# Kernel optimization log

Measured on AMD Instinct MI355X. Metric: run time of the kernel, lower is better.

The kernel has to match this reference:

```python
import jax, jax.numpy as jnp
import numpy as np

B, C, H, W = 32, 256, 32, 32
NUM_EMB = 1024
BETA = 0.25  # commitment_loss_weight


def setup_inputs() -> dict:
    key = jax.random.key(0)
    k_u, k_cb = jax.random.split(key)
    u = jax.random.normal(k_u, (B, C, H, W), dtype=jnp.float32)
    # kaiming_normal_ fan_in, relu: std = sqrt(2 / fan_in), fan_in = embedding_dim
    cb_std = float(np.sqrt(2.0 / C))
    codebook = jax.random.normal(k_cb, (NUM_EMB, C), dtype=jnp.float32) * cb_std
    return {"u": u, "codebook": codebook}


def reference(u, codebook):
    # u: [B, C, H, W] -> flat: [B*H*W, C]
    flat = jnp.transpose(u, (0, 2, 3, 1)).reshape(-1, C)
    # squared euclidean distances (argmin-equivalent to torch.cdist)
    d = (
        jnp.sum(flat * flat, axis=1, keepdims=True)
        - 2.0 * flat @ codebook.T
        + jnp.sum(codebook * codebook, axis=1)[None, :]
    )  # [B*H*W, NUM_EMB]
    encoding_indices = jnp.argmin(d, axis=1)  # [B*H*W]
    z_q = codebook[encoding_indices].reshape(B, H, W, C)
    z_q = jnp.transpose(z_q, (0, 3, 1, 2))  # [B, C, H, W]
    # straight-through (note: z_q is NOT detached here, matching the source)
    z_train = z_q + (u - jax.lax.stop_gradient(u))
    codebook_loss = jnp.mean((z_q - jax.lax.stop_gradient(u)) ** 2)
    commitment_loss = jnp.mean((u - jax.lax.stop_gradient(z_q)) ** 2)
    vq_loss = codebook_loss + BETA * commitment_loss
    return u, z_train, vq_loss, encoding_indices.reshape(B, H, W)
```

## Files before the change

kernel.cpp:

```cpp
#include <hip/hip_runtime.h>
#include <hip/hip_bf16.h>

#define BATCH 32
#define CHN   256
#define HWSZ  1024
#define NPIX  32768
#define NEMB  1024
#define NELEM 8388608
#define FLT_BIG 3.402823466e+38f

#define WS_CBT   0
#define WS_CNORM 262144
#define WS_XNORM 263168
#define WS_ACCUM 295936

#define OUT_U    0
#define OUT_ZT   8388608
#define OUT_LOSS 16777216
#define OUT_IDX  16777217

__device__ __forceinline__ void gld_lds16(const float* g, float* lds) {
    __builtin_amdgcn_global_load_lds(
        (const __attribute__((address_space(1))) void*)g,
        (__attribute__((address_space(3))) void*)lds, 16, 0, 0);
}

__global__ __launch_bounds__(256) void k_prep_cb(const float* __restrict__ cb,
                                                 float* __restrict__ ws) {
    int n = blockIdx.x;
    int c = threadIdx.x;
    float v = cb[(size_t)n * CHN + c];
    ws[WS_CBT + (size_t)c * NEMB + n] = v;
    float s = v * v;
    #pragma unroll
    for (int off = 32; off > 0; off >>= 1) s += __shfl_down(s, off, 64);
    __shared__ float ls[4];
    int w = threadIdx.x >> 6;
    if ((threadIdx.x & 63) == 0) ls[w] = s;
    __syncthreads();
    if (threadIdx.x == 0) ws[WS_CNORM + n] = (ls[0] + ls[1]) + (ls[2] + ls[3]);
}

__global__ __launch_bounds__(256) void k_prep_x(const float* __restrict__ u,
                                                float* __restrict__ ws) {
    int P0   = blockIdx.x * 64;
    int b    = P0 / HWSZ;
    int hw0  = P0 % HWSZ;
    int lane = threadIdx.x & 63;
    int grp  = threadIdx.x >> 6;
    const float* up = u + (size_t)b * CHN * HWSZ + hw0 + lane;
    float s = 0.f;
    int cbase = grp * 64;
    #pragma unroll 8
    for (int c = 0; c < 64; ++c) {
        float v = up[(size_t)(cbase + c) * HWSZ];
        s = fmaf(v, v, s);
    }
    __shared__ float ls[4][64];
    ls[grp][lane] = s;
    __syncthreads();
    if (grp == 0) {
        float x = (ls[0][lane] + ls[1][lane]) + (ls[2][lane] + ls[3][lane]);
        ws[WS_XNORM + P0 + lane] = x;
    }
    if (blockIdx.x == 0 && threadIdx.x == 0)
        *(double*)&ws[WS_ACCUM] = 0.0;
}

__global__ __launch_bounds__(256, 2) void k_argmin(const float* __restrict__ u,
                                                   const float* __restrict__ ws,
                                                   float* __restrict__ out_idx) {
    __shared__ float s_u[2][32][64];
    __shared__ float s_cb[2][32][256];

    const float* cbT   = ws + WS_CBT;
    const float* cnorm = ws + WS_CNORM;
    const float* xnorm = ws + WS_XNORM;

    int T   = blockIdx.x;
    int P0  = T * 64;
    int b   = P0 / HWSZ;
    int hw0 = P0 % HWSZ;
    int tid = threadIdx.x;
    int tx  = tid & 7;
    int ty  = tid >> 3;

    const float* ub = u + (size_t)b * CHN * HWSZ + hw0;

    int uq0_k  = tid >> 4;
    int uq0_p  = (tid & 15) << 2;
    int uq1_k  = (256 + tid) >> 4;
    int uq1_p  = (tid & 15) << 2;
    int cb_k0  = tid >> 6;
    int cb_j   = (tid & 63) << 2;

    float xn[8];
    #pragma unroll
    for (int i = 0; i < 8; ++i) xn[i] = xnorm[P0 + tx * 8 + i];

    float dmin[8];
    int   imin[8];
    #pragma unroll
    for (int i = 0; i < 8; ++i) { dmin[i] = FLT_BIG; imin[i] = 0; }

    auto stage = [&](int s, int buf) {
        int nt = s >> 3;
        int kc = s & 7;
        int n0 = nt * 256;
        int c0 = kc * 32;
        float* su  = &s_u[buf][0][0];
        float* scb = &s_cb[buf][0][0];
        gld_lds16(&ub[(size_t)(c0 + uq0_k) * HWSZ + uq0_p], &su[tid * 4]);
        gld_lds16(&ub[(size_t)(c0 + uq1_k) * HWSZ + uq1_p], &su[(256 + tid) * 4]);
        #pragma unroll
        for (int it = 0; it < 8; ++it) {
            int k = cb_k0 + it * 4;
            gld_lds16(&cbT[(size_t)(c0 + k) * NEMB + n0 + cb_j],
                      &scb[(it * 256 + tid) * 4]);
        }
    };

    stage(0, 0);

    for (int nt = 0; nt < 4; ++nt) {
        int n0 = nt * 256;
        float acc[8][8];
        #pragma unroll
        for (int i = 0; i < 8; ++i)
            #pragma unroll
            for (int j = 0; j < 8; ++j) acc[i][j] = 0.f;

        for (int kc = 0; kc < 8; ++kc) {
            int s   = nt * 8 + kc;
            int buf = s & 1;
            __syncthreads();
            if (s < 31) stage(s + 1, buf ^ 1);
            const float* su  = &s_u[buf][0][0];
            const float* scb = &s_cb[buf][0][0];
            #pragma unroll 8
            for (int k = 0; k < 32; ++k) {
                float4 a0 = *(const float4*)&su[k * 64 + tx * 8];
                float4 a1 = *(const float4*)&su[k * 64 + tx * 8 + 4];
                float4 b0 = *(const float4*)&scb[k * 256 + ty * 8];
                float4 b1 = *(const float4*)&scb[k * 256 + ty * 8 + 4];
                float a[8]; float bb[8];
                a[0]=a0.x; a[1]=a0.y; a[2]=a0.z; a[3]=a0.w;
                a[4]=a1.x; a[5]=a1.y; a[6]=a1.z; a[7]=a1.w;
                bb[0]=b0.x; bb[1]=b0.y; bb[2]=b0.z; bb[3]=b0.w;
                bb[4]=b1.x; bb[5]=b1.y; bb[6]=b1.z; bb[7]=b1.w;
                #pragma unroll
                for (int i = 0; i < 8; ++i)
                    #pragma unroll
                    for (int j = 0; j < 8; ++j)
                        acc[i][j] = fmaf(a[i], bb[j], acc[i][j]);
            }
        }
        float cn[8];
        #pragma unroll
        for (int j = 0; j < 8; ++j) cn[j] = cnorm[n0 + ty * 8 + j];
        #pragma unroll
        for (int i = 0; i < 8; ++i) {
            #pragma unroll
            for (int j = 0; j < 8; ++j) {
                float t1 = xn[i] - 2.0f * acc[i][j];
                float d  = t1 + cn[j];
                int   n  = n0 + ty * 8 + j;
                if (d < dmin[i]) { dmin[i] = d; imin[i] = n; }
            }
        }
    }

    __syncthreads();
    float* red_d = &s_cb[0][0][0];
    int*   red_i = (int*)&s_cb[0][8][0];
    #pragma unroll
    for (int i = 0; i < 8; ++i) {
        red_d[(tx * 8 + i) * 32 + ty] = dmin[i];
        red_i[(tx * 8 + i) * 32 + ty] = imin[i];
    }
    __syncthreads();
    if (tid < 64) {
        float bd = FLT_BIG; int bi = 0x7fffffff;
        #pragma unroll
        for (int t = 0; t < 32; ++t) {
            float d = red_d[tid * 32 + t];
            int   n = red_i[tid * 32 + t];
            if (d < bd || (d == bd && n < bi)) { bd = d; bi = n; }
        }
        out_idx[P0 + tid] = (float)bi;
    }
}

__global__ __launch_bounds__(256) void k_out(const float* __restrict__ u,
                                             const float* __restrict__ cb,
                                             const float* __restrict__ idxf,
                                             float* __restrict__ out,
                                             double* __restrict__ accum) {
    int P0   = blockIdx.x * 64;
    int b    = P0 / HWSZ;
    int hw0  = P0 % HWSZ;
    int lane = threadIdx.x & 63;
    int grp  = threadIdx.x >> 6;
    int p    = P0 + lane;
    int idx  = (int)idxf[p];
    const float* ub    = u + (size_t)b * CHN * HWSZ + hw0 + lane;
    float*       o0    = out + OUT_U  + (size_t)b * CHN * HWSZ + hw0 + lane;
    float*       o1    = out + OUT_ZT + (size_t)b * CHN * HWSZ + hw0 + lane;
    const float* cbrow = cb + (size_t)idx * CHN;
    float s = 0.f;
    #pragma unroll
    for (int r = 0; r < 8; ++r) {
        int c0 = grp * 8 + r * 32;
        float4 z0 = *(const float4*)&cbrow[c0];
        float4 z1 = *(const float4*)&cbrow[c0 + 4];
        float zq[8];
        zq[0]=z0.x; zq[1]=z0.y; zq[2]=z0.z; zq[3]=z0.w;
        zq[4]=z1.x; zq[5]=z1.y; zq[6]=z1.z; zq[7]=z1.w;
        #pragma unroll
        for (int cc = 0; cc < 8; ++cc) {
            int c = c0 + cc;
            float uv = ub[(size_t)c * HWSZ];
            float zv = zq[cc];
            o0[(size_t)c * HWSZ] = uv;
            o1[(size_t)c * HWSZ] = zv;
            float df = zv - uv;
            s = fmaf(df, df, s);
        }
    }
    #pragma unroll
    for (int off = 32; off > 0; off >>= 1) s += __shfl_down(s, off, 64);
    __shared__ float ls[4];
    if (lane == 0) ls[grp] = s;
    __syncthreads();
    if (threadIdx.x == 0) {
        float tot = (ls[0] + ls[1]) + (ls[2] + ls[3]);
        atomicAdd(accum, (double)tot);
    }
}

__global__ void k_loss(const double* __restrict__ accum,
                       float* __restrict__ out_loss) {
    float m = (float)(*accum / (double)NELEM);
    out_loss[0] = m + 0.25f * m;
}

extern "C" void kernel_launch(void* const* d_in, const int* in_sizes, int n_in,
                              void* d_out, int out_size, void* d_ws, size_t ws_size,
                              hipStream_t stream) {
    const float* u  = (const float*)d_in[0];
    const float* cb = (const float*)d_in[1];
    float* out = (float*)d_out;
    float* ws  = (float*)d_ws;

    k_prep_cb<<<dim3(NEMB),      dim3(256), 0, stream>>>(cb, ws);
    k_prep_x <<<dim3(NPIX / 64), dim3(256), 0, stream>>>(u, ws);
    k_argmin <<<dim3(NPIX / 64), dim3(256), 0, stream>>>(u, ws, out + OUT_IDX);
    k_out    <<<dim3(NPIX / 64), dim3(256), 0, stream>>>(u, cb, out + OUT_IDX, out,
                                                         (double*)(ws + WS_ACCUM));
    k_loss   <<<dim3(1),         dim3(1),   0, stream>>>((const double*)(ws + WS_ACCUM),
                                                         out + OUT_LOSS);
}
```

Baseline: 326.3 us.

## Split argmin over codebook quarters with 128-pixel tiles and atomic 64-bit min keys

The argmin kernel now uses 128-pixel by 256-codeword tiles, with each block handling one quarter of the codebook and a 16x8 register accumulator per thread. Partial minima are merged across blocks with a 64-bit atomicMin on packed (distance bits, index) keys, and the output kernel unpacks the index. The two prep kernels are fused into one launch that also initializes the keys. This aims to raise FMA reuse per LDS load and give the grid more blocks, at the cost of register pressure and global atomics. The packed key compares raw float bits, which orders correctly only for non-negative distances, so a slightly negative distance from rounding could be mis-ranked.

Result: slower. 820.1 us (+151.3%).

```diff
diff --git a/kernel.cpp b/kernel.cpp
--- a/kernel.cpp
+++ b/kernel.cpp
@@ -8,11 +8,13 @@
 #define NEMB  1024
 #define NELEM 8388608
 #define FLT_BIG 3.402823466e+38f
+#define KCH   16
 
 #define WS_CBT   0
 #define WS_CNORM 262144
 #define WS_XNORM 263168
-#define WS_ACCUM 295936
+#define WS_KEYS  296192
+#define WS_ACCUM 361728
 
 #define OUT_U    0
 #define OUT_ZT   8388608
@@ -25,187 +27,170 @@
         (__attribute__((address_space(3))) void*)lds, 16, 0, 0);
 }
 
-__global__ __launch_bounds__(256) void k_prep_cb(const float* __restrict__ cb,
-                                                 float* __restrict__ ws) {
-    int n = blockIdx.x;
-    int c = threadIdx.x;
-    float v = cb[(size_t)n * CHN + c];
-    ws[WS_CBT + (size_t)c * NEMB + n] = v;
-    float s = v * v;
-    #pragma unroll
-    for (int off = 32; off > 0; off >>= 1) s += __shfl_down(s, off, 64);
-    __shared__ float ls[4];
-    int w = threadIdx.x >> 6;
-    if ((threadIdx.x & 63) == 0) ls[w] = s;
+__global__ __launch_bounds__(256) void k_prep(const float* __restrict__ cb,
+                                              const float* __restrict__ u,
+                                              float* __restrict__ ws) {
+    int bid = blockIdx.x;
+    if (bid < NEMB) {
+        int n = bid;
+        int c = threadIdx.x;
+        float v = cb[(size_t)n * CHN + c];
+        ws[WS_CBT + (size_t)c * NEMB + n] = v;
+        float s = v * v;
+        #pragma unroll
+        for (int off = 32; off > 0; off >>= 1) s += __shfl_down(s, off, 64);
+        __shared__ float ls[4];
+        if ((threadIdx.x & 63) == 0) ls[threadIdx.x >> 6] = s;
+        __syncthreads();
+        if (threadIdx.x == 0) ws[WS_CNORM + n] = (ls[0] + ls[1]) + (ls[2] + ls[3]);
+    } else {
+        int pb  = bid - NEMB;
+        int P0  = pb * 64;
+        int b   = P0 >> 10;
+        int hw0 = P0 & 1023;
+        int lane = threadIdx.x & 63;
+        int grp  = threadIdx.x >> 6;
+        const float* up = u + (size_t)b * (CHN * HWSZ) + hw0 + lane;
+        float s = 0.f;
+        #pragma unroll 8
+        for (int c = 0; c < 64; ++c) {
+            float v = up[(size_t)(grp * 64 + c) * HWSZ];
+            s = fmaf(v, v, s);
+        }
+        __shared__ float ls2[4][64];
+        ls2[grp][lane] = s;
+        __syncthreads();
+        if (grp == 0)
+            ws[WS_XNORM + P0 + lane] =
+                (ls2[0][lane] + ls2[1][lane]) + (ls2[2][lane] + ls2[3][lane]);
+        if (threadIdx.x < 64)
+            ((unsigned long long*)(ws + WS_KEYS))[P0 + threadIdx.x] = ~0ULL;
+        if (pb == 0 && threadIdx.x == 0) *(double*)&ws[WS_ACCUM] = 0.0;
+    }
+}
+
+__global__ __launch_bounds__(256, 3) void k_argmin(const float* __restrict__ u,
+                                                   const float* __restrict__ ws,
+                                                   unsigned long long* __restrict__ keys) {
+    __shared__ float s_u[2][KCH * 128];
+    __shared__ float s_cb[2][KCH * 256];
+
+    const float* cbT = ws + WS_CBT;
+    int bid  = blockIdx.x;
+    int pb   = bid >> 2;
+    int part = bid & 3;
+    int P0   = pb * 128;
+    int b    = P0 >> 10;
+    int hw0  = P0 & 1023;
+    int tid  = threadIdx.x;
+    int tx   = tid & 7;
+    int ty   = tid >> 3;
+    int n0   = part * 256;
+    const float* ub = u + (size_t)b * (CHN * HWSZ) + hw0;
+
+    const int qa0 = tid, qa1 = tid + 256;
+
+    auto stage = [&](int s, int buf) {
+        int c0 = s * KCH;
+        float* su  = &s_u[buf][0];
+        float* scb = &s_cb[buf][0];
+        gld_lds16(&ub[(size_t)(c0 + (qa0 >> 5)) * HWSZ + (qa0 & 31) * 4], &su[qa0 * 4]);
+        gld_lds16(&ub[(size_t)(c0 + (qa1 >> 5)) * HWSZ + (qa1 & 31) * 4], &su[qa1 * 4]);
+        #pragma unroll
+        for (int it = 0; it < 4; ++it) {
+            int q = it * 256 + tid;
+            gld_lds16(&cbT[(size_t)(c0 + (q >> 6)) * NEMB + n0 + (q & 63) * 4],
+                      &scb[q * 4]);
+        }
+    };
+
+    float acc[16][8];
+    #pragma unroll
+    for (int i = 0; i < 16; ++i)
+        #pragma unroll
+        for (int j = 0; j < 8; ++j) acc[i][j] = 0.f;
+
+    stage(0, 0);
+
+    for (int s = 0; s < 16; ++s) {
+        int buf = s & 1;
+        __syncthreads();
+        if (s < 15) stage(s + 1, buf ^ 1);
+        const float* su  = &s_u[buf][0];
+        const float* scb = &s_cb[buf][0];
+        #pragma unroll
+        for (int k = 0; k < KCH; ++k) {
+            float4 t0 = *(const float4*)&su[(k * 32 + 0 * 8 + tx) * 4];
+            float4 t1 = *(const float4*)&su[(k * 32 + 1 * 8 + tx) * 4];
+            float4 t2 = *(const float4*)&su[(k * 32 + 2 * 8 + tx) * 4];
+            float4 t3 = *(const float4*)&su[(k * 32 + 3 * 8 + tx) * 4];
+            float4 b0 = *(const float4*)&scb[k * 256 + ty * 8];
+            float4 b1 = *(const float4*)&scb[k * 256 + ty * 8 + 4];
+            float a[16] = {t0.x,t0.y,t0.z,t0.w, t1.x,t1.y,t1.z,t1.w,
+                           t2.x,t2.y,t2.z,t2.w, t3.x,t3.y,t3.z,t3.w};
+            float bb[8] = {b0.x,b0.y,b0.z,b0.w, b1.x,b1.y,b1.z,b1.w};
+            #pragma unroll
+            for (int i = 0; i < 16; ++i)
+                #pragma unroll
+                for (int j = 0; j < 8; ++j)
+                    acc[i][j] = fmaf(a[i], bb[j], acc[i][j]);
+        }
+    }
+
     __syncthreads();
-    if (threadIdx.x == 0) ws[WS_CNORM + n] = (ls[0] + ls[1]) + (ls[2] + ls[3]);
-}
-
-__global__ __launch_bounds__(256) void k_prep_x(const float* __restrict__ u,
-                                                float* __restrict__ ws) {
-    int P0   = blockIdx.x * 64;
-    int b    = P0 / HWSZ;
-    int hw0  = P0 % HWSZ;
-    int lane = threadIdx.x & 63;
-    int grp  = threadIdx.x >> 6;
-    const float* up = u + (size_t)b * CHN * HWSZ + hw0 + lane;
-    float s = 0.f;
-    int cbase = grp * 64;
-    #pragma unroll 8
-    for (int c = 0; c < 64; ++c) {
-        float v = up[(size_t)(cbase + c) * HWSZ];
-        s = fmaf(v, v, s);
-    }
-    __shared__ float ls[4][64];
-    ls[grp][lane] = s;
-    __syncthreads();
-    if (grp == 0) {
-        float x = (ls[0][lane] + ls[1][lane]) + (ls[2][lane] + ls[3][lane]);
-        ws[WS_XNORM + P0 + lane] = x;
-    }
-    if (blockIdx.x == 0 && threadIdx.x == 0)
-        *(double*)&ws[WS_ACCUM] = 0.0;
-}
-
-__global__ __launch_bounds__(256, 2) void k_argmin(const float* __restrict__ u,
-                                                   const float* __restrict__ ws,
-                                                   float* __restrict__ out_idx) {
-    __shared__ float s_u[2][32][64];
-    __shared__ float s_cb[2][32][256];
-
-    const float* cbT   = ws + WS_CBT;
+
     const float* cnorm = ws + WS_CNORM;
     const float* xnorm = ws + WS_XNORM;
-
-    int T   = blockIdx.x;
-    int P0  = T * 64;
-    int b   = P0 / HWSZ;
-    int hw0 = P0 % HWSZ;
-    int tid = threadIdx.x;
-    int tx  = tid & 7;
-    int ty  = tid >> 3;
-
-    const float* ub = u + (size_t)b * CHN * HWSZ + hw0;
-
-    int uq0_k  = tid >> 4;
-    int uq0_p  = (tid & 15) << 2;
-    int uq1_k  = (256 + tid) >> 4;
-    int uq1_p  = (tid & 15) << 2;
-    int cb_k0  = tid >> 6;
-    int cb_j   = (tid & 63) << 2;
-
-    float xn[8];
-    #pragma unroll
-    for (int i = 0; i < 8; ++i) xn[i] = xnorm[P0 + tx * 8 + i];
-
-    float dmin[8];
-    int   imin[8];
-    #pragma unroll
-    for (int i = 0; i < 8; ++i) { dmin[i] = FLT_BIG; imin[i] = 0; }
-
-    auto stage = [&](int s, int buf) {
-        int nt = s >> 3;
-        int kc = s & 7;
-        int n0 = nt * 256;
-        int c0 = kc * 32;
-        float* su  = &s_u[buf][0][0];
-        float* scb = &s_cb[buf][0][0];
-        gld_lds16(&ub[(size_t)(c0 + uq0_k) * HWSZ + uq0_p], &su[tid * 4]);
-        gld_lds16(&ub[(size_t)(c0 + uq1_k) * HWSZ + uq1_p], &su[(256 + tid) * 4]);
-        #pragma unroll
-        for (int it = 0; it < 8; ++it) {
-            int k = cb_k0 + it * 4;
-            gld_lds16(&cbT[(size_t)(c0 + k) * NEMB + n0 + cb_j],
-                      &scb[(it * 256 + tid) * 4]);
-        }
-    };
-
-    stage(0, 0);
-
-    for (int nt = 0; nt < 4; ++nt) {
-        int n0 = nt * 256;
-        float acc[8][8];
-        #pragma unroll
-        for (int i = 0; i < 8; ++i)
-            #pragma unroll
-            for (int j = 0; j < 8; ++j) acc[i][j] = 0.f;
-
-        for (int kc = 0; kc < 8; ++kc) {
-            int s   = nt * 8 + kc;
-            int buf = s & 1;
-            __syncthreads();
-            if (s < 31) stage(s + 1, buf ^ 1);
-            const float* su  = &s_u[buf][0][0];
-            const float* scb = &s_cb[buf][0][0];
-            #pragma unroll 8
-            for (int k = 0; k < 32; ++k) {
-                float4 a0 = *(const float4*)&su[k * 64 + tx * 8];
-                float4 a1 = *(const float4*)&su[k * 64 + tx * 8 + 4];
-                float4 b0 = *(const float4*)&scb[k * 256 + ty * 8];
-                float4 b1 = *(const float4*)&scb[k * 256 + ty * 8 + 4];
-                float a[8]; float bb[8];
-                a[0]=a0.x; a[1]=a0.y; a[2]=a0.z; a[3]=a0.w;
-                a[4]=a1.x; a[5]=a1.y; a[6]=a1.z; a[7]=a1.w;
-                bb[0]=b0.x; bb[1]=b0.y; bb[2]=b0.z; bb[3]=b0.w;
-                bb[4]=b1.x; bb[5]=b1.y; bb[6]=b1.z; bb[7]=b1.w;
-                #pragma unroll
-                for (int i = 0; i < 8; ++i)
-                    #pragma unroll
-                    for (int j = 0; j < 8; ++j)
-                        acc[i][j] = fmaf(a[i], bb[j], acc[i][j]);
-            }
-        }
-        float cn[8];
-        #pragma unroll
-        for (int j = 0; j < 8; ++j) cn[j] = cnorm[n0 + ty * 8 + j];
-        #pragma unroll
-        for (int i = 0; i < 8; ++i) {
-            #pragma unroll
-            for (int j = 0; j < 8; ++j) {
-                float t1 = xn[i] - 2.0f * acc[i][j];
-                float d  = t1 + cn[j];
-                int   n  = n0 + ty * 8 + j;
-                if (d < dmin[i]) { dmin[i] = d; imin[i] = n; }
-            }
-        }
-    }
-
+    float cn[8];
+    #pragma unroll
+    for (int j = 0; j < 8; ++j) cn[j] = cnorm[n0 + ty * 8 + j];
+    float* red_d = &s_cb[0][0];
+    int*   red_i = (int*)&s_cb[1][0];
+    #pragma unroll
+    for (int i = 0; i < 16; ++i) {
+        int pix = (tx + (i >> 2) * 8) * 4 + (i & 3);
+        float x  = xnorm[P0 + pix];
+        float bd = FLT_BIG; int bi = 0;
+        #pragma unroll
+        for (int j = 0; j < 8; ++j) {
+            float t1 = x - 2.0f * acc[i][j];
+            float d  = t1 + cn[j];
+            if (d < bd) { bd = d; bi = ty * 8 + j; }
+        }
+        red_d[ty * 128 + pix] = bd;
+        red_i[ty * 128 + pix] = bi;
+    }
     __syncthreads();
-    float* red_d = &s_cb[0][0][0];
-    int*   red_i = (int*)&s_cb[0][8][0];
-    #pragma unroll
-    for (int i = 0; i < 8; ++i) {
-        red_d[(tx * 8 + i) * 32 + ty] = dmin[i];
-        red_i[(tx * 8 + i) * 32 + ty] = imin[i];
-    }
-    __syncthreads();
-    if (tid < 64) {
-        float bd = FLT_BIG; int bi = 0x7fffffff;
-        #pragma unroll
+    if (tid < 128) {
+        float bd = FLT_BIG; int bi = 0;
+        #pragma unroll 8
         for (int t = 0; t < 32; ++t) {
-            float d = red_d[tid * 32 + t];
-            int   n = red_i[tid * 32 + t];
-            if (d < bd || (d == bd && n < bi)) { bd = d; bi = n; }
-        }
-        out_idx[P0 + tid] = (float)bi;
+            float d = red_d[t * 128 + tid];
+            int   n = red_i[t * 128 + tid];
+            if (d < bd) { bd = d; bi = n; }
+        }
+        unsigned long long key =
+            ((unsigned long long)__float_as_uint(bd) << 32) | (unsigned)(n0 + bi);
+        atomicMin(&keys[P0 + tid], key);
     }
 }
 
 __global__ __launch_bounds__(256) void k_out(const float* __restrict__ u,
                                              const float* __restrict__ cb,
-                                             const float* __restrict__ idxf,
+                                             const unsigned long long* __restrict__ keys,
                                              float* __restrict__ out,
                                              double* __restrict__ accum) {
     int P0   = blockIdx.x * 64;
-    int b    = P0 / HWSZ;
-    int hw0  = P0 % HWSZ;
+    int b    = P0 >> 10;
+    int hw0  = P0 & 1023;
     int lane = threadIdx.x & 63;
     int grp  = threadIdx.x >> 6;
     int p    = P0 + lane;
-    int idx  = (int)idxf[p];
-    const float* ub    = u + (size_t)b * CHN * HWSZ + hw0 + lane;
-    float*       o0    = out + OUT_U  + (size_t)b * CHN * HWSZ + hw0 + lane;
-    float*       o1    = out + OUT_ZT + (size_t)b * CHN * HWSZ + hw0 + lane;
+    unsigned long long key = keys[p];
+    int idx  = (int)(unsigned int)(key & 0xffffffffull);
+    const float* ub    = u + (size_t)b * (CHN * HWSZ) + hw0 + lane;
+    float*       o0    = out + OUT_U  + (size_t)b * (CHN * HWSZ) + hw0 + lane;
+    float*       o1    = out + OUT_ZT + (size_t)b * (CHN * HWSZ) + hw0 + lane;
     const float* cbrow = cb + (size_t)idx * CHN;
     float s = 0.f;
     #pragma unroll
@@ -213,9 +198,7 @@
         int c0 = grp * 8 + r * 32;
         float4 z0 = *(const float4*)&cbrow[c0];
         float4 z1 = *(const float4*)&cbrow[c0 + 4];
-        float zq[8];
-        zq[0]=z0.x; zq[1]=z0.y; zq[2]=z0.z; zq[3]=z0.w;
-        zq[4]=z1.x; zq[5]=z1.y; zq[6]=z1.z; zq[7]=z1.w;
+        float zq[8] = {z0.x,z0.y,z0.z,z0.w, z1.x,z1.y,z1.z,z1.w};
         #pragma unroll
         for (int cc = 0; cc < 8; ++cc) {
             int c = c0 + cc;
@@ -236,6 +219,7 @@
         float tot = (ls[0] + ls[1]) + (ls[2] + ls[3]);
         atomicAdd(accum, (double)tot);
     }
+    if (grp == 0) out[OUT_IDX + p] = (float)idx;
 }
 
 __global__ void k_loss(const double* __restrict__ accum,
@@ -252,11 +236,12 @@
     float* out = (float*)d_out;
     float* ws  = (float*)d_ws;
 
-    k_prep_cb<<<dim3(NEMB),      dim3(256), 0, stream>>>(cb, ws);
-    k_prep_x <<<dim3(NPIX / 64), dim3(256), 0, stream>>>(u, ws);
-    k_argmin <<<dim3(NPIX / 64), dim3(256), 0, stream>>>(u, ws, out + OUT_IDX);
-    k_out    <<<dim3(NPIX / 64), dim3(256), 0, stream>>>(u, cb, out + OUT_IDX, out,
-                                                         (double*)(ws + WS_ACCUM));
-    k_loss   <<<dim3(1),         dim3(1),   0, stream>>>((const double*)(ws + WS_ACCUM),
-                                                         out + OUT_LOSS);
-}
+    k_prep  <<<dim3(NEMB + NPIX / 64), dim3(256), 0, stream>>>(cb, u, ws);
+    k_argmin<<<dim3(1024),             dim3(256), 0, stream>>>(u, ws,
+                 (unsigned long long*)(ws + WS_KEYS));
+    k_out   <<<dim3(NPIX / 64),        dim3(256), 0, stream>>>(u, cb,
+                 (const unsigned long long*)(ws + WS_KEYS), out,
+                 (double*)(ws + WS_ACCUM));
+    k_loss  <<<dim3(1),                dim3(1),   0, stream>>>(
+                 (const double*)(ws + WS_ACCUM), out + OUT_LOSS);
+}
```
